# Performance work log

Hardware: AMD Instinct MI355X
Metric: run time of the kernel (lower is better)

## Reference

```python
import jax, jax.numpy as jnp
import numpy as np

N_NODES = 100000
N_EDGES = 800000
HIDDEN = 128


def setup_inputs() -> dict:
    key = jax.random.key(0)
    ks = jax.random.split(key, 9)
    h_n = jax.random.normal(ks[0], (N_NODES, HIDDEN), dtype=jnp.float32)
    edge_src = jax.random.randint(ks[1], (N_EDGES,), 0, N_NODES, dtype=jnp.int32)
    edge_dst = jax.random.randint(ks[2], (N_EDGES,), 0, N_NODES, dtype=jnp.int32)
    s = 0.05
    W_w = jax.random.normal(ks[3], (HIDDEN, HIDDEN), dtype=jnp.float32) * s
    W_b = jax.random.normal(ks[4], (HIDDEN,), dtype=jnp.float32) * s
    Ws_w = jax.random.normal(ks[5], (HIDDEN, HIDDEN), dtype=jnp.float32) * s
    Ws_b = jax.random.normal(ks[6], (HIDDEN,), dtype=jnp.float32) * s
    Wt_w = jax.random.normal(ks[7], (HIDDEN, HIDDEN), dtype=jnp.float32) * s
    Wt_b = jax.random.normal(ks[8], (HIDDEN,), dtype=jnp.float32) * s
    return {"h_n": h_n, "edge_src": edge_src, "edge_dst": edge_dst,
            "W_w": W_w, "W_b": W_b, "Ws_w": Ws_w, "Ws_b": Ws_b,
            "Wt_w": Wt_w, "Wt_b": Wt_b}


def reference(h_n, edge_src, edge_dst, W_w, W_b, Ws_w, Ws_b, Wt_w, Wt_b):
    # Dense linears (nn.Linear: x @ W.T + b)
    Wh = h_n @ W_w.T + W_b        # [N,H] used for A @ W(h)
    Wsh = h_n @ Ws_w.T + Ws_b     # [N,H] self term
    Wth = h_n @ Wt_w.T + Wt_b     # [N,H] used for A.T @ W_trans(h)
    # A[src,dst] = 1:  (A @ X)[i]   = sum over edges (i,j) of X[j]
    #              (A.T @ X)[j] = sum over edges (i,j) of X[i]
    agg_fwd = jax.ops.segment_sum(Wh[edge_dst], edge_src, num_segments=N_NODES)
    agg_bwd = jax.ops.segment_sum(Wth[edge_src], edge_dst, num_segments=N_NODES)
    return jax.nn.relu(agg_fwd + Wsh + agg_bwd)
```

## Files before the change

### kernel.cpp

```cpp
#include <hip/hip_runtime.h>
#include <hip/hip_bf16.h>

#define NN 100000
#define NE 800000
#define HIDDEN 128
#define NED (2 * NE)
#define BKN 64
#define NBF 1563
#define NBUCK (2 * NBF)
#define PS 13
#define CHUNK 8192
#define PBLK ((NED + CHUNK - 1) / CHUNK)
#define NTILES 3125

typedef __attribute__((ext_vector_type(8))) short bf16x8;
typedef __attribute__((ext_vector_type(4))) short bf16x4;
typedef __attribute__((ext_vector_type(4))) float f32x4;

__device__ __forceinline__ short f2bf(float f) {
  union { float f; unsigned u; } x; x.f = f;
  unsigned r = x.u + 0x7fffu + ((x.u >> 16) & 1u);
  return (short)(r >> 16);
}
__device__ __forceinline__ float bf2f(short s) {
  union { unsigned u; float f; } x;
  x.u = ((unsigned)(unsigned short)s) << 16;
  return x.f;
}

__global__ __launch_bounds__(256) void convert_weights(
    const float* __restrict__ m0, const float* __restrict__ m1,
    const float* __restrict__ m2, short* __restrict__ out) {
  int i = blockIdx.x * 256 + threadIdx.x;
  int m = i >> 14, j = i & 16383;
  const float* s = (m == 0) ? m0 : (m == 1) ? m1 : m2;
  out[i] = f2bf(s[j]);
}

__global__ __launch_bounds__(256) void convert_h(
    const float* __restrict__ h, short* __restrict__ h_bf) {
  int i = blockIdx.x * 256 + threadIdx.x;
  f32x4 v = *(const f32x4*)(h + (size_t)i * 4);
  bf16x4 o;
#pragma unroll
  for (int j = 0; j < 4; j++) o[j] = f2bf(v[j]);
  *(bf16x4*)(h_bf + (size_t)i * 4) = o;
}

__global__ __launch_bounds__(256) void part_count(
    const int* __restrict__ esrc, const int* __restrict__ edst,
    int* __restrict__ ghist) {
  __shared__ int lh[NBUCK];
  int tid = threadIdx.x;
  for (int i = tid; i < NBUCK; i += 256) lh[i] = 0;
  __syncthreads();
  int base = blockIdx.x * CHUNK;
  int nit = min(CHUNK, NED - base);
  for (int k = tid; k < nit; k += 256) {
    int ed = base + k;
    int b;
    if (ed < NE) b = esrc[ed] >> 6;
    else b = NBF + (edst[ed - NE] >> 6);
    atomicAdd(&lh[b], 1);
  }
  __syncthreads();
  for (int i = tid; i < NBUCK; i += 256) {
    int c = lh[i];
    if (c) atomicAdd(ghist + i, c);
  }
}

__global__ __launch_bounds__(1024) void bucket_scan(
    const int* __restrict__ ghist, int* __restrict__ bstart,
    int* __restrict__ gcur) {
  __shared__ int lds[1024];
  __shared__ int carry;
  int tid = threadIdx.x;
  if (tid == 0) carry = 0;
  __syncthreads();
  for (int t = 0; t < 4; t++) {
    int i = t * 1024 + tid;
    int v = (i < NBUCK) ? ghist[i] : 0;
    lds[tid] = v;
    __syncthreads();
    for (int off = 1; off < 1024; off <<= 1) {
      int x = lds[tid];
      int add = (tid >= off) ? lds[tid - off] : 0;
      __syncthreads();
      lds[tid] = x + add;
      __syncthreads();
    }
    int excl = lds[tid] - v + carry;
    if (i < NBUCK) { bstart[i] = excl; gcur[i] = excl; }
    int tot = lds[1023];
    __syncthreads();
    if (tid == 0) carry += tot;
    __syncthreads();
  }
  if (tid == 0) bstart[NBUCK] = carry;
}

__global__ __launch_bounds__(256) void part_scatter(
    const int* __restrict__ esrc, const int* __restrict__ edst,
    int* __restrict__ gcur, unsigned* __restrict__ ELP) {
  __shared__ int lh[NBUCK];
  __shared__ int loff[NBUCK];
  __shared__ int lcur[NBUCK];
  __shared__ int gbase[NBUCK];
  __shared__ int psum[256];
  __shared__ unsigned buf[CHUNK];
  __shared__ unsigned short bidA[CHUNK];
  int tid = threadIdx.x;
  for (int i = tid; i < NBUCK; i += 256) lh[i] = 0;
  __syncthreads();
  int base = blockIdx.x * CHUNK;
  int nit = min(CHUNK, NED - base);
  for (int k = tid; k < nit; k += 256) {
    int ed = base + k;
    int b;
    if (ed < NE) b = esrc[ed] >> 6;
    else b = NBF + (edst[ed - NE] >> 6);
    atomicAdd(&lh[b], 1);
  }
  __syncthreads();
  int s = 0;
  int lo0 = tid * PS, hi0 = min(NBUCK, tid * PS + PS);
  for (int j = lo0; j < hi0; j++) s += lh[j];
  psum[tid] = s;
  __syncthreads();
  for (int off = 1; off < 256; off <<= 1) {
    int x = psum[tid];
    int add = (tid >= off) ? psum[tid - off] : 0;
    __syncthreads();
    psum[tid] = x + add;
    __syncthreads();
  }
  int run = psum[tid] - s;
  for (int j = lo0; j < hi0; j++) { loff[j] = run; lcur[j] = run; run += lh[j]; }
  __syncthreads();
  for (int b = tid; b < NBUCK; b += 256) {
    int c = lh[b];
    if (c) gbase[b] = atomicAdd(gcur + b, c);
  }
  __syncthreads();
  for (int k = tid; k < nit; k += 256) {
    int ed = base + k;
    int b, tl, nbr;
    if (ed < NE) { int tg = esrc[ed]; nbr = edst[ed]; b = tg >> 6; tl = tg & 63; }
    else { int e = ed - NE; int tg = edst[e]; nbr = esrc[e]; b = NBF + (tg >> 6); tl = tg & 63; }
    int slot = atomicAdd(&lcur[b], 1);
    buf[slot] = ((unsigned)tl << 17) | (unsigned)nbr;
    bidA[slot] = (unsigned short)b;
  }
  __syncthreads();
  for (int i = tid; i < nit; i += 256) {
    int b = bidA[i];
    ELP[gbase[b] + (i - loff[b])] = buf[i];
  }
}

#define ACC8(V) { a0f+=bf2f((V)[0]); a1f+=bf2f((V)[1]); a2f+=bf2f((V)[2]); a3f+=bf2f((V)[3]); \
                  a4f+=bf2f((V)[4]); a5f+=bf2f((V)[5]); a6f+=bf2f((V)[6]); a7f+=bf2f((V)[7]); }
#define MACC8(M,V) { a0f=fmaf(M,bf2f((V)[0]),a0f); a1f=fmaf(M,bf2f((V)[1]),a1f); \
                     a2f=fmaf(M,bf2f((V)[2]),a2f); a3f=fmaf(M,bf2f((V)[3]),a3f); \
                     a4f=fmaf(M,bf2f((V)[4]),a4f); a5f=fmaf(M,bf2f((V)[5]),a5f); \
                     a6f=fmaf(M,bf2f((V)[6]),a6f); a7f=fmaf(M,bf2f((V)[7]),a7f); }
__global__ __launch_bounds__(256, 6) void bucket_gather(
    const short* __restrict__ h_bf, const unsigned* __restrict__ ELP,
    const int* __restrict__ bstart,
    short* __restrict__ aggF, short* __restrict__ aggB,
    int* __restrict__ degFB) {
  __shared__ int sorted[1024];
  __shared__ int cnt[BKN];
  __shared__ int pfx[BKN];
  __shared__ int cur[BKN];
  int tid = threadIdx.x;
  int blk = blockIdx.x;
  int s = bstart[blk], e = bstart[blk + 1], n = e - s;
  if (tid < BKN) cnt[tid] = 0;
  __syncthreads();
  for (int k = tid; k < n; k += 256) atomicAdd(&cnt[ELP[s + k] >> 17], 1);
  __syncthreads();
  int v = (tid < BKN) ? cnt[tid] : 0;
  if (tid < BKN) pfx[tid] = v;
  __syncthreads();
  for (int off = 1; off < BKN; off <<= 1) {
    int add = (tid < BKN && tid >= off) ? pfx[tid - off] : 0;
    __syncthreads();
    if (tid < BKN) pfx[tid] += add;
    __syncthreads();
  }
  if (tid < BKN) cur[tid] = pfx[tid] - cnt[tid];
  __syncthreads();
  for (int k = tid; k < n; k += 256) {
    unsigned pv = ELP[s + k];
    int slot = atomicAdd(&cur[pv >> 17], 1);
    sorted[slot] = (int)(pv & 0x1FFFFu);
  }
  __syncthreads();
  int dir = blk >= NBF;
  int node0 = (dir ? blk - NBF : blk) * BKN;
  short* agg = dir ? aggB : aggF;
  int qw = tid >> 4, q = tid & 15;
  const short* hb = h_bf + (size_t)q * 8;
#pragma unroll
  for (int t = 0; t < 4; t++) {
    int nd = qw * 4 + t;
    int b0 = pfx[nd];
    int deg = cnt[nd];
    int a0 = b0 - deg;
    float a0f = 0.f, a1f = 0.f, a2f = 0.f, a3f = 0.f;
    float a4f = 0.f, a5f = 0.f, a6f = 0.f, a7f = 0.f;
    if (deg > 0) {
      int lastp = b0 - 1;
      int i0 = sorted[a0];
      int i1 = sorted[min(a0 + 1, lastp)];
      int i2 = sorted[min(a0 + 2, lastp)];
      int i3 = sorted[min(a0 + 3, lastp)];
      bf16x8 v0 = *(const bf16x8*)(hb + (size_t)i0 * HIDDEN);
      bf16x8 v1 = *(const bf16x8*)(hb + (size_t)i1 * HIDDEN);
      bf16x8 v2 = *(const bf16x8*)(hb + (size_t)i2 * HIDDEN);
      bf16x8 v3 = *(const bf16x8*)(hb + (size_t)i3 * HIDDEN);
      int j = a0;
      int ni0 = sorted[min(j + 4, lastp)];
      int ni1 = sorted[min(j + 5, lastp)];
      int ni2 = sorted[min(j + 6, lastp)];
      int ni3 = sorted[min(j + 7, lastp)];
      while (j + 4 <= b0) {
        ACC8(v0); v0 = *(const bf16x8*)(hb + (size_t)ni0 * HIDDEN);
        ACC8(v1); v1 = *(const bf16x8*)(hb + (size_t)ni1 * HIDDEN);
        ACC8(v2); v2 = *(const bf16x8*)(hb + (size_t)ni2 * HIDDEN);
        ACC8(v3); v3 = *(const bf16x8*)(hb + (size_t)ni3 * HIDDEN);
        j += 4;
        ni0 = sorted[min(j + 4, lastp)];
        ni1 = sorted[min(j + 5, lastp)];
        ni2 = sorted[min(j + 6, lastp)];
        ni3 = sorted[min(j + 7, lastp)];
      }
      int r = b0 - j;
      float m1 = (r > 0) ? 1.f : 0.f;
      float m2 = (r > 1) ? 1.f : 0.f;
      float m3 = (r > 2) ? 1.f : 0.f;
      MACC8(m1, v0); MACC8(m2, v1); MACC8(m3, v2);
    }
    int node = node0 + nd;
    if (node < NN) {
      bf16x8 o;
      o[0] = f2bf(a0f); o[1] = f2bf(a1f); o[2] = f2bf(a2f); o[3] = f2bf(a3f);
      o[4] = f2bf(a4f); o[5] = f2bf(a5f); o[6] = f2bf(a6f); o[7] = f2bf(a7f);
      *(bf16x8*)(agg + (size_t)node * HIDDEN + q * 8) = o;
    }
  }
  if (tid < BKN) {
    int node = node0 + tid;
    if (node < NN) degFB[dir * NN + node] = cnt[tid];
  }
}

__global__ __launch_bounds__(512, 4) void gemm_fused(
    const short* __restrict__ h_bf, const short* __restrict__ aggF,
    const short* __restrict__ aggB, const short* __restrict__ Wbf,
    const float* __restrict__ Wb, const float* __restrict__ Wsb,
    const float* __restrict__ Wtb, const int* __restrict__ degFB,
    float* __restrict__ out) {
  __shared__ short At[3 * 32 * 136];
  int tid = threadIdx.x;
  int lane = tid & 63;
  int m16 = lane & 15;
  int kq  = lane >> 4;
  int col0 = (tid >> 6) * 16;

  bf16x8 wf[3][4];
#pragma unroll
  for (int i = 0; i < 3; i++)
#pragma unroll
    for (int t = 0; t < 4; t++)
      wf[i][t] = *(const bf16x8*)(Wbf + i * 16384 + (col0 + m16) * 128 + t * 32 + kq * 8);

  f32x4 bW = *(const f32x4*)(Wb  + col0 + kq * 4);
  f32x4 bS = *(const f32x4*)(Wsb + col0 + kq * 4);
  f32x4 bT = *(const f32x4*)(Wtb + col0 + kq * 4);

  int srow = tid >> 4, skc = tid & 15;
  const short* mats[3] = { h_bf, aggF, aggB };
  const short* gbs[3];
  short* lps[3];
#pragma unroll
  for (int k = 0; k < 3; k++) {
    gbs[k] = mats[k] + srow * 128 + skc * 8;
    lps[k] = At + k * 4352 + srow * 136 + skc * 8;
  }

  int tile = blockIdx.x;
  bf16x8 ld[3];
#pragma unroll
  for (int k = 0; k < 3; k++)
    ld[k] = *(const bf16x8*)(gbs[k] + (size_t)tile * 4096);

  while (tile < NTILES) {
    int row0 = tile * 32;
    __syncthreads();
#pragma unroll
    for (int k = 0; k < 3; k++) *(bf16x8*)lps[k] = ld[k];
    __syncthreads();
    int ntile = tile + gridDim.x;
    if (ntile < NTILES) {
#pragma unroll
      for (int k = 0; k < 3; k++)
        ld[k] = *(const bf16x8*)(gbs[k] + (size_t)ntile * 4096);
    }
#pragma unroll
    for (int g = 0; g < 2; g++) {
      f32x4 acc = {0.f, 0.f, 0.f, 0.f};
      const short* lb = At + (g * 16 + m16) * 136 + kq * 8;
#pragma unroll
      for (int i = 0; i < 3; i++)
#pragma unroll
        for (int t = 0; t < 4; t++) {
          bf16x8 af = *(const bf16x8*)(lb + i * 4352 + t * 32);
          acc = __builtin_amdgcn_mfma_f32_16x16x32_bf16(wf[i][t], af, acc, 0, 0, 0);
        }
      int r = row0 + g * 16 + m16;
      float dF = (float)degFB[r];
      float dB = (float)degFB[NN + r];
      f32x4 v;
#pragma unroll
      for (int j = 0; j < 4; j++)
        v[j] = fmaxf(acc[j] + bS[j] + dF * bW[j] + dB * bT[j], 0.f);
      *(f32x4*)(out + (size_t)r * HIDDEN + col0 + kq * 4) = v;
    }
    tile = ntile;
  }
}

extern "C" void kernel_launch(void* const* d_in, const int* in_sizes, int n_in,
                              void* d_out, int out_size, void* d_ws, size_t ws_size,
                              hipStream_t stream) {
  const float* h    = (const float*)d_in[0];
  const int*   esrc = (const int*)d_in[1];
  const int*   edst = (const int*)d_in[2];
  const float* Ww   = (const float*)d_in[3];
  const float* Wb   = (const float*)d_in[4];
  const float* Wsw  = (const float*)d_in[5];
  const float* Wsb  = (const float*)d_in[6];
  const float* Wtw  = (const float*)d_in[7];
  const float* Wtb  = (const float*)d_in[8];
  float* out = (float*)d_out;

  char* ws = (char*)d_ws;
  int*      ghist  = (int*)(ws + 0);
  int*      bstart = (int*)(ws + 12544);
  int*      gcur   = (int*)(ws + 25088);
  unsigned* ELP    = (unsigned*)(ws + 37632);
  short*    Wbf    = (short*)(ws + 6437632);
  short*    h_bf   = (short*)(ws + 6535936);
  short*    aggF   = (short*)(ws + 32135936);
  short*    aggB   = (short*)(ws + 57735936);
  int*      degFB  = (int*)(ws + 83335936);

  hipMemsetAsync(ghist, 0, NBUCK * sizeof(int), stream);

  convert_weights<<<192, 256, 0, stream>>>(Wsw, Ww, Wtw, Wbf);
  convert_h<<<12500, 256, 0, stream>>>(h, h_bf);
  part_count<<<PBLK, 256, 0, stream>>>(esrc, edst, ghist);
  bucket_scan<<<1, 1024, 0, stream>>>(ghist, bstart, gcur);
  part_scatter<<<PBLK, 256, 0, stream>>>(esrc, edst, gcur, ELP);
  bucket_gather<<<NBUCK, 256, 0, stream>>>(h_bf, ELP, bstart, aggF, aggB, degFB);
  gemm_fused<<<1024, 512, 0, stream>>>(
      h_bf, aggF, aggB, Wbf, Wb, Wsb, Wtb, degFB, out);
}
```

Baseline: 264.4 us.

## Stage gathered neighbor rows through double-buffered LDS in bucket gather

The bucket_gather kernel now loads neighbor rows cooperatively in chunks of 128 sorted edges into a double-buffered LDS row buffer, prefetching the next chunk while accumulating the current one from LDS. Before, each thread issued dependent global gathers per node. The aim is to keep more independent global loads in flight and balance uneven node degrees across the block, at the cost of about 70KB of LDS, occupancy lowered to 2 blocks per SIMD, and a barrier per chunk. Separately, part_scatter halves CHUNK to 4096 and drops one LDS array by reusing lcur, which reduces its LDS footprint and should allow more concurrent blocks.

```diff
diff --git a/kernel.cpp b/kernel.cpp
--- a/kernel.cpp
+++ b/kernel.cpp
@@ -9,8 +9,9 @@
 #define NBF 1563
 #define NBUCK (2 * NBF)
 #define PS 13
-#define CHUNK 8192
+#define CHUNK 4096
 #define PBLK ((NED + CHUNK - 1) / CHUNK)
+#define GC 128
 #define NTILES 3125
 
 typedef __attribute__((ext_vector_type(8))) short bf16x8;
@@ -103,15 +104,14 @@
 __global__ __launch_bounds__(256) void part_scatter(
     const int* __restrict__ esrc, const int* __restrict__ edst,
     int* __restrict__ gcur, unsigned* __restrict__ ELP) {
-  __shared__ int lh[NBUCK];
+  __shared__ int lcur[NBUCK];
   __shared__ int loff[NBUCK];
-  __shared__ int lcur[NBUCK];
   __shared__ int gbase[NBUCK];
   __shared__ int psum[256];
   __shared__ unsigned buf[CHUNK];
   __shared__ unsigned short bidA[CHUNK];
   int tid = threadIdx.x;
-  for (int i = tid; i < NBUCK; i += 256) lh[i] = 0;
+  for (int i = tid; i < NBUCK; i += 256) lcur[i] = 0;
   __syncthreads();
   int base = blockIdx.x * CHUNK;
   int nit = min(CHUNK, NED - base);
@@ -120,12 +120,12 @@
     int b;
     if (ed < NE) b = esrc[ed] >> 6;
     else b = NBF + (edst[ed - NE] >> 6);
-    atomicAdd(&lh[b], 1);
+    atomicAdd(&lcur[b], 1);
   }
   __syncthreads();
   int s = 0;
   int lo0 = tid * PS, hi0 = min(NBUCK, tid * PS + PS);
-  for (int j = lo0; j < hi0; j++) s += lh[j];
+  for (int j = lo0; j < hi0; j++) s += lcur[j];
   psum[tid] = s;
   __syncthreads();
   for (int off = 1; off < 256; off <<= 1) {
@@ -136,11 +136,12 @@
     __syncthreads();
   }
   int run = psum[tid] - s;
-  for (int j = lo0; j < hi0; j++) { loff[j] = run; lcur[j] = run; run += lh[j]; }
+  for (int j = lo0; j < hi0; j++) { loff[j] = run; run += lcur[j]; }
   __syncthreads();
   for (int b = tid; b < NBUCK; b += 256) {
-    int c = lh[b];
+    int c = lcur[b];
     if (c) gbase[b] = atomicAdd(gcur + b, c);
+    lcur[b] = loff[b];
   }
   __syncthreads();
   for (int k = tid; k < nit; k += 256) {
@@ -159,13 +160,16 @@
   }
 }
 
-#define ACC8(V) { a0f+=bf2f((V)[0]); a1f+=bf2f((V)[1]); a2f+=bf2f((V)[2]); a3f+=bf2f((V)[3]); \
-                  a4f+=bf2f((V)[4]); a5f+=bf2f((V)[5]); a6f+=bf2f((V)[6]); a7f+=bf2f((V)[7]); }
-#define MACC8(M,V) { a0f=fmaf(M,bf2f((V)[0]),a0f); a1f=fmaf(M,bf2f((V)[1]),a1f); \
-                     a2f=fmaf(M,bf2f((V)[2]),a2f); a3f=fmaf(M,bf2f((V)[3]),a3f); \
-                     a4f=fmaf(M,bf2f((V)[4]),a4f); a5f=fmaf(M,bf2f((V)[5]),a5f); \
-                     a6f=fmaf(M,bf2f((V)[6]),a6f); a7f=fmaf(M,bf2f((V)[7]),a7f); }
-__global__ __launch_bounds__(256, 6) void bucket_gather(
+#define ACCU(u, V) { ac[u][0]+=bf2f((V)[0]); ac[u][1]+=bf2f((V)[1]); \
+                     ac[u][2]+=bf2f((V)[2]); ac[u][3]+=bf2f((V)[3]); \
+                     ac[u][4]+=bf2f((V)[4]); ac[u][5]+=bf2f((V)[5]); \
+                     ac[u][6]+=bf2f((V)[6]); ac[u][7]+=bf2f((V)[7]); }
+#define MACCU(u, M, V) { ac[u][0]=fmaf(M,bf2f((V)[0]),ac[u][0]); ac[u][1]=fmaf(M,bf2f((V)[1]),ac[u][1]); \
+                         ac[u][2]=fmaf(M,bf2f((V)[2]),ac[u][2]); ac[u][3]=fmaf(M,bf2f((V)[3]),ac[u][3]); \
+                         ac[u][4]=fmaf(M,bf2f((V)[4]),ac[u][4]); ac[u][5]=fmaf(M,bf2f((V)[5]),ac[u][5]); \
+                         ac[u][6]=fmaf(M,bf2f((V)[6]),ac[u][6]); ac[u][7]=fmaf(M,bf2f((V)[7]),ac[u][7]); }
+#define LROW(SL) (*(const bf16x8*)(rb + (size_t)((SL) - s0) * 136 + q * 8))
+__global__ __launch_bounds__(256, 2) void bucket_gather(
     const short* __restrict__ h_bf, const unsigned* __restrict__ ELP,
     const int* __restrict__ bstart,
     short* __restrict__ aggF, short* __restrict__ aggB,
@@ -174,6 +178,7 @@
   __shared__ int cnt[BKN];
   __shared__ int pfx[BKN];
   __shared__ int cur[BKN];
+  __shared__ short rowbuf[2 * GC * 136];
   int tid = threadIdx.x;
   int blk = blockIdx.x;
   int s = bstart[blk], e = bstart[blk + 1], n = e - s;
@@ -198,56 +203,102 @@
     sorted[slot] = (int)(pv & 0x1FFFFu);
   }
   __syncthreads();
+
+  int qw = tid >> 4, q = tid & 15;
+  float ac[4][8];
+#pragma unroll
+  for (int u = 0; u < 4; u++)
+#pragma unroll
+    for (int j = 0; j < 8; j++) ac[u][j] = 0.f;
+
+  int a0[4], b0[4];
+#pragma unroll
+  for (int u = 0; u < 4; u++) {
+    int nd = qw * 4 + u;
+    b0[u] = pfx[nd];
+    a0[u] = b0[u] - cnt[nd];
+  }
+
+  int nc = (n + GC - 1) / GC;
+  bf16x8 st[8];
+  if (n > 0) {
+#pragma unroll
+    for (int k = 0; k < 8; k++) {
+      int r = qw + k * 16;
+      int nbr = sorted[min(r, n - 1)];
+      st[k] = *(const bf16x8*)(h_bf + (size_t)nbr * HIDDEN + q * 8);
+    }
+#pragma unroll
+    for (int k = 0; k < 8; k++) {
+      int r = qw + k * 16;
+      *(bf16x8*)(rowbuf + r * 136 + q * 8) = st[k];
+    }
+  }
+  __syncthreads();
+
+  for (int c = 0; c < nc; c++) {
+    int s0 = c * GC;
+    int bsel = c & 1;
+    int s1 = s0 + GC;
+    int more = (s1 < n);
+    if (more) {
+#pragma unroll
+      for (int k = 0; k < 8; k++) {
+        int r = qw + k * 16;
+        int nbr = sorted[min(s1 + r, n - 1)];
+        st[k] = *(const bf16x8*)(h_bf + (size_t)nbr * HIDDEN + q * 8);
+      }
+    }
+    int cend = min(n, s1);
+    const short* rb = rowbuf + bsel * (GC * 136);
+#pragma unroll
+    for (int u = 0; u < 4; u++) {
+      int lo = max(a0[u], s0);
+      int hi = min(b0[u], cend);
+      if (lo < hi) {
+        int lastp = hi - 1;
+        bf16x8 v0 = LROW(lo);
+        bf16x8 v1 = LROW(min(lo + 1, lastp));
+        bf16x8 v2 = LROW(min(lo + 2, lastp));
+        bf16x8 v3 = LROW(min(lo + 3, lastp));
+        int j = lo;
+        while (j + 4 <= hi) {
+          ACCU(u, v0); v0 = LROW(min(j + 4, lastp));
+          ACCU(u, v1); v1 = LROW(min(j + 5, lastp));
+          ACCU(u, v2); v2 = LROW(min(j + 6, lastp));
+          ACCU(u, v3); v3 = LROW(min(j + 7, lastp));
+          j += 4;
+        }
+        int rr = hi - j;
+        float m1 = (rr > 0) ? 1.f : 0.f;
+        float m2 = (rr > 1) ? 1.f : 0.f;
+        float m3 = (rr > 2) ? 1.f : 0.f;
+        MACCU(u, m1, v0); MACCU(u, m2, v1); MACCU(u, m3, v2);
+      }
+    }
+    if (more) {
+      short* wb = rowbuf + (1 - bsel) * (GC * 136);
+#pragma unroll
+      for (int k = 0; k < 8; k++) {
+        int r = qw + k * 16;
+        *(bf16x8*)(wb + r * 136 + q * 8) = st[k];
+      }
+    }
+    __syncthreads();
+  }
+
   int dir = blk >= NBF;
   int node0 = (dir ? blk - NBF : blk) * BKN;
   short* agg = dir ? aggB : aggF;
-  int qw = tid >> 4, q = tid & 15;
-  const short* hb = h_bf + (size_t)q * 8;
-#pragma unroll
-  for (int t = 0; t < 4; t++) {
-    int nd = qw * 4 + t;
-    int b0 = pfx[nd];
-    int deg = cnt[nd];
-    int a0 = b0 - deg;
-    float a0f = 0.f, a1f = 0.f, a2f = 0.f, a3f = 0.f;
-    float a4f = 0.f, a5f = 0.f, a6f = 0.f, a7f = 0.f;
-    if (deg > 0) {
-      int lastp = b0 - 1;
-      int i0 = sorted[a0];
-      int i1 = sorted[min(a0 + 1, lastp)];
-      int i2 = sorted[min(a0 + 2, lastp)];
-      int i3 = sorted[min(a0 + 3, lastp)];
-      bf16x8 v0 = *(const bf16x8*)(hb + (size_t)i0 * HIDDEN);
-      bf16x8 v1 = *(const bf16x8*)(hb + (size_t)i1 * HIDDEN);
-      bf16x8 v2 = *(const bf16x8*)(hb + (size_t)i2 * HIDDEN);
-      bf16x8 v3 = *(const bf16x8*)(hb + (size_t)i3 * HIDDEN);
-      int j = a0;
-      int ni0 = sorted[min(j + 4, lastp)];
-      int ni1 = sorted[min(j + 5, lastp)];
-      int ni2 = sorted[min(j + 6, lastp)];
-      int ni3 = sorted[min(j + 7, lastp)];
-      while (j + 4 <= b0) {
-        ACC8(v0); v0 = *(const bf16x8*)(hb + (size_t)ni0 * HIDDEN);
-        ACC8(v1); v1 = *(const bf16x8*)(hb + (size_t)ni1 * HIDDEN);
-        ACC8(v2); v2 = *(const bf16x8*)(hb + (size_t)ni2 * HIDDEN);
-        ACC8(v3); v3 = *(const bf16x8*)(hb + (size_t)ni3 * HIDDEN);
-        j += 4;
-        ni0 = sorted[min(j + 4, lastp)];
-        ni1 = sorted[min(j + 5, lastp)];
-        ni2 = sorted[min(j + 6, lastp)];
-        ni3 = sorted[min(j + 7, lastp)];
-      }
-      int r = b0 - j;
-      float m1 = (r > 0) ? 1.f : 0.f;
-      float m2 = (r > 1) ? 1.f : 0.f;
-      float m3 = (r > 2) ? 1.f : 0.f;
-      MACC8(m1, v0); MACC8(m2, v1); MACC8(m3, v2);
-    }
-    int node = node0 + nd;
+#pragma unroll
+  for (int u = 0; u < 4; u++) {
+    int node = node0 + qw * 4 + u;
     if (node < NN) {
       bf16x8 o;
-      o[0] = f2bf(a0f); o[1] = f2bf(a1f); o[2] = f2bf(a2f); o[3] = f2bf(a3f);
-      o[4] = f2bf(a4f); o[5] = f2bf(a5f); o[6] = f2bf(a6f); o[7] = f2bf(a7f);
+      o[0] = f2bf(ac[u][0]); o[1] = f2bf(ac[u][1]);
+      o[2] = f2bf(ac[u][2]); o[3] = f2bf(ac[u][3]);
+      o[4] = f2bf(ac[u][4]); o[5] = f2bf(ac[u][5]);
+      o[6] = f2bf(ac[u][6]); o[7] = f2bf(ac[u][7]);
       *(bf16x8*)(agg + (size_t)node * HIDDEN + q * 8) = o;
     }
   }
```

After: 298.8 us. +13.0%, slower.

## Halve partition chunk, shrink scatter LDS, and use wave-shuffle bucket scan

Applied to the files above, without the earlier changes.

Halves the edge chunk per partition block, which doubles the number of blocks in the histogram and scatter passes. The scatter kernel now reuses the histogram array as its cursor array, which removes one bucket-sized LDS array and should let more blocks fit per CU. The single-block bucket scan is rewritten to have each thread own four buckets and use wave shuffles, replacing a barrier-heavy LDS Hillis-Steele scan over four rounds. Smaller chunks mean more global atomics on the bucket cursors and less per-block locality.

```diff
diff --git a/kernel.cpp b/kernel.cpp
--- a/kernel.cpp
+++ b/kernel.cpp
@@ -9,7 +9,7 @@
 #define NBF 1563
 #define NBUCK (2 * NBF)
 #define PS 13
-#define CHUNK 8192
+#define CHUNK 4096
 #define PBLK ((NED + CHUNK - 1) / CHUNK)
 #define NTILES 3125
 
@@ -73,45 +73,58 @@
 __global__ __launch_bounds__(1024) void bucket_scan(
     const int* __restrict__ ghist, int* __restrict__ bstart,
     int* __restrict__ gcur) {
-  __shared__ int lds[1024];
-  __shared__ int carry;
-  int tid = threadIdx.x;
-  if (tid == 0) carry = 0;
-  __syncthreads();
-  for (int t = 0; t < 4; t++) {
-    int i = t * 1024 + tid;
-    int v = (i < NBUCK) ? ghist[i] : 0;
-    lds[tid] = v;
-    __syncthreads();
-    for (int off = 1; off < 1024; off <<= 1) {
-      int x = lds[tid];
-      int add = (tid >= off) ? lds[tid - off] : 0;
-      __syncthreads();
-      lds[tid] = x + add;
-      __syncthreads();
-    }
-    int excl = lds[tid] - v + carry;
-    if (i < NBUCK) { bstart[i] = excl; gcur[i] = excl; }
-    int tot = lds[1023];
-    __syncthreads();
-    if (tid == 0) carry += tot;
-    __syncthreads();
-  }
-  if (tid == 0) bstart[NBUCK] = carry;
+  __shared__ int wsum[16];
+  __shared__ int woff[16];
+  int tid = threadIdx.x;
+  int lane = tid & 63, wv = tid >> 6;
+  int base = tid * 4;
+  int v0 = (base + 0 < NBUCK) ? ghist[base + 0] : 0;
+  int v1 = (base + 1 < NBUCK) ? ghist[base + 1] : 0;
+  int v2 = (base + 2 < NBUCK) ? ghist[base + 2] : 0;
+  int v3 = (base + 3 < NBUCK) ? ghist[base + 3] : 0;
+  int s = v0 + v1 + v2 + v3;
+  int inc = s;
+#pragma unroll
+  for (int d = 1; d < 64; d <<= 1) {
+    int t = __shfl_up(inc, d, 64);
+    if (lane >= d) inc += t;
+  }
+  if (lane == 63) wsum[wv] = inc;
+  __syncthreads();
+  if (wv == 0) {
+    int x = (lane < 16) ? wsum[lane] : 0;
+    int i2 = x;
+#pragma unroll
+    for (int d = 1; d < 16; d <<= 1) {
+      int t = __shfl_up(i2, d, 64);
+      if (lane >= d) i2 += t;
+    }
+    if (lane < 16) woff[lane] = i2 - x;
+  }
+  __syncthreads();
+  int e = woff[wv] + inc - s;
+  if (base + 0 < NBUCK) { bstart[base + 0] = e; gcur[base + 0] = e; }
+  e += v0;
+  if (base + 1 < NBUCK) { bstart[base + 1] = e; gcur[base + 1] = e; }
+  e += v1;
+  if (base + 2 < NBUCK) { bstart[base + 2] = e; gcur[base + 2] = e; }
+  e += v2;
+  if (base + 3 < NBUCK) { bstart[base + 3] = e; gcur[base + 3] = e; }
+  e += v3;
+  if (tid == 1023) bstart[NBUCK] = e;
 }
 
 __global__ __launch_bounds__(256) void part_scatter(
     const int* __restrict__ esrc, const int* __restrict__ edst,
     int* __restrict__ gcur, unsigned* __restrict__ ELP) {
-  __shared__ int lh[NBUCK];
+  __shared__ int lcur[NBUCK];
   __shared__ int loff[NBUCK];
-  __shared__ int lcur[NBUCK];
   __shared__ int gbase[NBUCK];
   __shared__ int psum[256];
   __shared__ unsigned buf[CHUNK];
   __shared__ unsigned short bidA[CHUNK];
   int tid = threadIdx.x;
-  for (int i = tid; i < NBUCK; i += 256) lh[i] = 0;
+  for (int i = tid; i < NBUCK; i += 256) lcur[i] = 0;
   __syncthreads();
   int base = blockIdx.x * CHUNK;
   int nit = min(CHUNK, NED - base);
@@ -120,12 +133,12 @@
     int b;
     if (ed < NE) b = esrc[ed] >> 6;
     else b = NBF + (edst[ed - NE] >> 6);
-    atomicAdd(&lh[b], 1);
+    atomicAdd(&lcur[b], 1);
   }
   __syncthreads();
   int s = 0;
   int lo0 = tid * PS, hi0 = min(NBUCK, tid * PS + PS);
-  for (int j = lo0; j < hi0; j++) s += lh[j];
+  for (int j = lo0; j < hi0; j++) s += lcur[j];
   psum[tid] = s;
   __syncthreads();
   for (int off = 1; off < 256; off <<= 1) {
@@ -136,11 +149,12 @@
     __syncthreads();
   }
   int run = psum[tid] - s;
-  for (int j = lo0; j < hi0; j++) { loff[j] = run; lcur[j] = run; run += lh[j]; }
+  for (int j = lo0; j < hi0; j++) { loff[j] = run; run += lcur[j]; }
   __syncthreads();
   for (int b = tid; b < NBUCK; b += 256) {
-    int c = lh[b];
+    int c = lcur[b];
     if (c) gbase[b] = atomicAdd(gcur + b, c);
+    lcur[b] = loff[b];
   }
   __syncthreads();
   for (int k = tid; k < nit; k += 256) {
```

Result: faster. 258.7 us (-2.2%).
